# Kernel optimization log

Hardware: AMD Instinct MI355X
Metric: run time of the kernel (lower is better)

Reference implementation:

```python
import jax, jax.numpy as jnp
import numpy as np

H, D = 8, 16          # heads, per-head dim (hidden 128 = H*D)
IN_C, HID, OUT_C = 128, 128, 64
NG, ND = 100000, 50000
EG, EDG = 800000, 800000
NEG_SLOPE = 0.2


def setup_inputs() -> dict:
    key = jax.random.key(0)
    ks = jax.random.split(key, 20)
    inp = {}
    inp['x_gene'] = jax.random.normal(ks[0], (NG, IN_C), jnp.float32)
    inp['x_disease'] = jax.random.normal(ks[1], (ND, IN_C), jnp.float32)
    inp['eg_src'] = jax.random.randint(ks[2], (EG,), 0, NG, jnp.int32)
    inp['eg_dst'] = jax.random.randint(ks[3], (EG,), 0, NG, jnp.int32)
    inp['edg_src'] = jax.random.randint(ks[4], (EDG,), 0, ND, jnp.int32)
    inp['edg_dst'] = jax.random.randint(ks[5], (EDG,), 0, NG, jnp.int32)
    s = 1.0 / np.sqrt(IN_C)
    inp['W_gene'] = jax.random.normal(ks[6], (IN_C, HID), jnp.float32) * s
    inp['b_gene'] = jnp.zeros((HID,), jnp.float32)
    inp['W_dis'] = jax.random.normal(ks[7], (IN_C, HID), jnp.float32) * s
    inp['b_dis'] = jnp.zeros((HID,), jnp.float32)
    inp['att_src_gg'] = jax.random.normal(ks[8], (H, D), jnp.float32) * 0.1
    inp['att_dst_gg'] = jax.random.normal(ks[9], (H, D), jnp.float32) * 0.1
    inp['att_src_dg'] = jax.random.normal(ks[10], (H, D), jnp.float32) * 0.1
    inp['att_dst_dg'] = jax.random.normal(ks[11], (H, D), jnp.float32) * 0.1
    inp['Wk'] = jax.random.normal(ks[12], (HID, HID), jnp.float32) * (1.0 / np.sqrt(HID))
    inp['bk'] = jnp.zeros((HID,), jnp.float32)
    inp['q'] = jax.random.normal(ks[13], (HID,), jnp.float32) * 0.1
    inp['W_lin'] = jax.random.normal(ks[14], (HID, OUT_C), jnp.float32) * (1.0 / np.sqrt(HID))
    inp['b_lin'] = jnp.zeros((OUT_C,), jnp.float32)
    return inp


def _edge_attn(xs, xd, src, dst, a_s, a_d, n_dst):
    # xs:[Ns,H,D] projected src feats, xd:[Nd,H,D]; GAT-style per-edge-type attention
    e_src = (xs * a_s).sum(-1)                      # [Ns,H]
    e_dst = (xd * a_d).sum(-1)                      # [Nd,H]
    alpha = jax.nn.leaky_relu(e_src[src] + e_dst[dst], NEG_SLOPE)   # [E,H]
    m = jax.ops.segment_max(alpha, dst, num_segments=n_dst)
    m = jnp.where(jnp.isfinite(m), m, 0.0)
    ex = jnp.exp(alpha - m[dst])
    denom = jax.ops.segment_sum(ex, dst, num_segments=n_dst)
    w = ex / (denom[dst] + 1e-16)                   # softmax over incoming edges
    msg = xs[src] * w[..., None]                    # [E,H,D]
    out = jax.ops.segment_sum(msg, dst, num_segments=n_dst)  # [Nd,H,D]
    return jax.nn.relu(out.reshape(n_dst, H * D))


def reference(x_gene, x_disease, eg_src, eg_dst, edg_src, edg_dst,
              W_gene, b_gene, W_dis, b_dis,
              att_src_gg, att_dst_gg, att_src_dg, att_dst_dg,
              Wk, bk, q, W_lin, b_lin):
    ng = x_gene.shape[0]
    hg = (x_gene @ W_gene + b_gene).reshape(ng, H, D)
    hd = (x_disease @ W_dis + b_dis).reshape(-1, H, D)
    # metapath aggregations landing on 'gene'
    out_gg = _edge_attn(hg, hg, eg_src, eg_dst, att_src_gg, att_dst_gg, ng)
    out_dg = _edge_attn(hd, hg, edg_src, edg_dst, att_src_dg, att_dst_dg, ng)
    outs = jnp.stack([out_gg, out_dg])              # [K=2, Ng, HID]
    # semantic-level attention
    score = (jnp.tanh(outs @ Wk + bk).mean(1) * q).sum(-1)   # [K]
    beta = jax.nn.softmax(score)
    gene = (beta[:, None, None] * outs).sum(0)      # [Ng, HID]
    return gene @ W_lin + b_lin                     # [Ng, OUT_C]
```

## Files before the change

### kernel.cpp

```cpp
#include <hip/hip_runtime.h>
#include <cstdint>
#include <cstddef>

#define NEG_SLOPE 0.2f
#define BSHIFT 8

typedef __attribute__((ext_vector_type(8))) short short8;
typedef __attribute__((ext_vector_type(4))) float f32x4;

__device__ __forceinline__ float leakyf(float x) { return x > 0.f ? x : NEG_SLOPE * x; }
__device__ __forceinline__ float fast_tanh(float x) {
    float e = __expf(2.f * x);
    return 1.f - 2.f / (e + 1.f);
}
__device__ __forceinline__ unsigned short f2bf(float x) {
    unsigned u = __float_as_uint(x);
    unsigned r = u + 0x7FFFu + ((u >> 16) & 1u);
    return (unsigned short)(r >> 16);
}

__global__ __launch_bounds__(256) void proj_kernel(
    const float* __restrict__ x, const float* __restrict__ W, const float* __restrict__ bias,
    unsigned short* __restrict__ hout, int N,
    const float* __restrict__ att0, float* __restrict__ e0,
    const float* __restrict__ att1, float* __restrict__ e1,
    const float* __restrict__ att2, float* __restrict__ e2)
{
    __shared__ float xlds[32 * 128];
    __shared__ float wlds[16 * 128];
    const int t = threadIdx.x;
    const int row0 = blockIdx.x * 32;
    #pragma unroll
    for (int p = 0; p < 4; ++p) {
        int idx = t + 256 * p;
        int r = idx >> 5;
        int c4 = idx & 31;
        float4 v = make_float4(0.f, 0.f, 0.f, 0.f);
        if (row0 + r < N) v = *(const float4*)(x + (size_t)(row0 + r) * 128 + c4 * 4);
        *(float4*)(xlds + r * 128 + c4 * 4) = v;
    }
    const int rg = t >> 5, ct = t & 31;
    float acc[4][4];
    {
        float4 bv = *(const float4*)(bias + ct * 4);
        #pragma unroll
        for (int rr = 0; rr < 4; ++rr) {
            acc[rr][0] = bv.x; acc[rr][1] = bv.y; acc[rr][2] = bv.z; acc[rr][3] = bv.w;
        }
    }
    for (int kc = 0; kc < 8; ++kc) {
        __syncthreads();
        #pragma unroll
        for (int p = 0; p < 2; ++p) {
            int idx = t + 256 * p;
            *(float4*)(wlds + idx * 4) = *(const float4*)(W + (size_t)kc * 2048 + idx * 4);
        }
        __syncthreads();
        #pragma unroll 2
        for (int i2 = 0; i2 < 16; i2 += 4) {
            const int i = kc * 16 + i2;
            float4 xv[4];
            #pragma unroll
            for (int rr = 0; rr < 4; ++rr) xv[rr] = *(const float4*)(xlds + (rg + 8 * rr) * 128 + i);
            #pragma unroll
            for (int qq = 0; qq < 4; ++qq) {
                float4 wv = *(const float4*)(wlds + (i2 + qq) * 128 + ct * 4);
                #pragma unroll
                for (int rr = 0; rr < 4; ++rr) {
                    float xs = ((const float*)&xv[rr])[qq];
                    acc[rr][0] = fmaf(xs, wv.x, acc[rr][0]);
                    acc[rr][1] = fmaf(xs, wv.y, acc[rr][1]);
                    acc[rr][2] = fmaf(xs, wv.z, acc[rr][2]);
                    acc[rr][3] = fmaf(xs, wv.w, acc[rr][3]);
                }
            }
        }
    }
    #pragma unroll
    for (int rr = 0; rr < 4; ++rr) {
        int grow = row0 + rg + 8 * rr;
        if (grow < N) {
            int2 u;
            u.x = (int)f2bf(acc[rr][0]) | ((int)f2bf(acc[rr][1]) << 16);
            u.y = (int)f2bf(acc[rr][2]) | ((int)f2bf(acc[rr][3]) << 16);
            *(int2*)(hout + (size_t)grow * 128 + ct * 4) = u;
        }
    }
    const int head = ct >> 2;
    const bool wlane = (ct & 3) == 0;
    if (att0) {
        float4 av = *(const float4*)(att0 + ct * 4);
        #pragma unroll
        for (int rr = 0; rr < 4; ++rr) {
            float p_ = acc[rr][0] * av.x + acc[rr][1] * av.y + acc[rr][2] * av.z + acc[rr][3] * av.w;
            p_ += __shfl_xor(p_, 1);
            p_ += __shfl_xor(p_, 2);
            int grow = row0 + rg + 8 * rr;
            if (wlane && grow < N) e0[(size_t)grow * 8 + head] = p_;
        }
    }
    if (att1) {
        float4 av = *(const float4*)(att1 + ct * 4);
        #pragma unroll
        for (int rr = 0; rr < 4; ++rr) {
            float p_ = acc[rr][0] * av.x + acc[rr][1] * av.y + acc[rr][2] * av.z + acc[rr][3] * av.w;
            p_ += __shfl_xor(p_, 1);
            p_ += __shfl_xor(p_, 2);
            int grow = row0 + rg + 8 * rr;
            if (wlane && grow < N) e1[(size_t)grow * 8 + head] = p_;
        }
    }
    if (att2) {
        float4 av = *(const float4*)(att2 + ct * 4);
        #pragma unroll
        for (int rr = 0; rr < 4; ++rr) {
            float p_ = acc[rr][0] * av.x + acc[rr][1] * av.y + acc[rr][2] * av.z + acc[rr][3] * av.w;
            p_ += __shfl_xor(p_, 1);
            p_ += __shfl_xor(p_, 2);
            int grow = row0 + rg + 8 * rr;
            if (wlane && grow < N) e2[(size_t)grow * 8 + head] = p_;
        }
    }
}

__global__ __launch_bounds__(256) void bucket_hist(
    const int* __restrict__ dstg, int Eg, const int* __restrict__ dstd, int Ed,
    int NBg, int NBtot, int* __restrict__ bucketCnt)
{
    __shared__ int h[1024];
    const int t = threadIdx.x;
    for (int j = t; j < NBtot; j += 256) h[j] = 0;
    __syncthreads();
    const int Etot = Eg + Ed;
    const int base = blockIdx.x * 4096;
    #pragma unroll
    for (int k = 0; k < 16; ++k) {
        int i = base + k * 256 + t;
        if (i < Etot) {
            int b = (i < Eg) ? (dstg[i] >> BSHIFT) : NBg + (dstd[i - Eg] >> BSHIFT);
            atomicAdd(&h[b], 1);
        }
    }
    __syncthreads();
    for (int j = t; j < NBtot; j += 256) {
        int c = h[j];
        if (c) atomicAdd(&bucketCnt[j], c);
    }
}

__global__ void bucket_scan(const int* __restrict__ bucketCnt, int NBtot, int Etot,
                            int* __restrict__ bucketBase, int* __restrict__ bucketCursor)
{
    __shared__ int s[1024];
    int t = threadIdx.x;
    int v = (t < NBtot) ? bucketCnt[t] : 0;
    s[t] = v;
    __syncthreads();
    for (int o = 1; o < 1024; o <<= 1) {
        int add = (t >= o) ? s[t - o] : 0;
        __syncthreads();
        s[t] += add;
        __syncthreads();
    }
    if (t < NBtot) {
        int e = s[t] - v;
        bucketBase[t] = e;
        bucketCursor[t] = e;
    }
    if (t == 0) bucketBase[NBtot] = Etot;
}

__global__ __launch_bounds__(256) void bucket_scatter(
    const int* __restrict__ dstg, const int* __restrict__ srcg, int Eg,
    const int* __restrict__ dstd, const int* __restrict__ srcd, int Ed,
    int NBg, int NBtot, int* __restrict__ bucketCursor, unsigned* __restrict__ coarse)
{
    __shared__ int h[800];
    __shared__ int basearr[800];
    __shared__ int cur[800];
    const int t = threadIdx.x;
    for (int j = t; j < NBtot; j += 256) h[j] = 0;
    __syncthreads();
    const int Etot = Eg + Ed;
    const int base = blockIdx.x * 4096;
    int bk[16];
    unsigned pk[16];
    #pragma unroll
    for (int k = 0; k < 16; ++k) {
        int i = base + k * 256 + t;
        bk[k] = -1;
        if (i < Etot) {
            int dst, src, goff;
            if (i < Eg) { dst = dstg[i]; src = srcg[i]; goff = 0; }
            else        { dst = dstd[i - Eg]; src = srcd[i - Eg]; goff = NBg; }
            bk[k] = goff + (dst >> BSHIFT);
            pk[k] = (unsigned)src | ((unsigned)(dst & 255) << 24);
            atomicAdd(&h[bk[k]], 1);
        }
    }
    __syncthreads();
    for (int j = t; j < NBtot; j += 256) {
        int c = h[j];
        basearr[j] = c ? atomicAdd(&bucketCursor[j], c) : 0;
        cur[j] = 0;
    }
    __syncthreads();
    #pragma unroll
    for (int k = 0; k < 16; ++k) {
        if (bk[k] >= 0) {
            int r = atomicAdd(&cur[bk[k]], 1);
            coarse[basearr[bk[k]] + r] = pk[k];
        }
    }
}

__global__ __launch_bounds__(256) void bucket_sort(
    const unsigned* __restrict__ coarse, const int* __restrict__ bucketBase,
    int NBg, int Eg, int Ed, int N,
    int* __restrict__ offg, int* __restrict__ offd,
    int* __restrict__ srcs_g, int* __restrict__ srcs_d)
{
    __shared__ int hist[256];
    __shared__ int excl[256];
    __shared__ int cur[256];
    const int b = blockIdx.x;
    const int t = threadIdx.x;
    const int s0 = bucketBase[b], s1 = bucketBase[b + 1];
    const int cnt = s1 - s0;
    const bool isg = b < NBg;
    const int d0 = (isg ? b : b - NBg) << BSHIFT;
    hist[t] = 0;
    __syncthreads();
    for (int i = t; i < cnt; i += 256) {
        unsigned p = coarse[s0 + i];
        atomicAdd(&hist[p >> 24], 1);
    }
    __syncthreads();
    int v = hist[t];
    excl[t] = v;
    __syncthreads();
    for (int o = 1; o < 256; o <<= 1) {
        int add = (t >= o) ? excl[t - o] : 0;
        __syncthreads();
        excl[t] += add;
        __syncthreads();
    }
    const int e = excl[t] - v;
    const int localBase = isg ? s0 : s0 - Eg;
    const int d = d0 + t;
    if (d < N) {
        if (isg) offg[d] = localBase + e;
        else     offd[d] = localBase + e;
    }
    cur[t] = e;
    __syncthreads();
    int* outp = isg ? srcs_g : srcs_d;
    for (int i = t; i < cnt; i += 256) {
        unsigned p = coarse[s0 + i];
        int r = atomicAdd(&cur[p >> 24], 1);
        outp[localBase + r] = (int)(p & 0xFFFFFFu);
    }
    if (b == 0 && t == 0) { offg[N] = Eg; offd[N] = Ed; }
}

__global__ __launch_bounds__(256) void aggregate_kernel(
    const unsigned short* __restrict__ xs,
    const float* __restrict__ esrc,
    const float* __restrict__ edst,
    const int* __restrict__ off,
    const int* __restrict__ srcsorted,
    float* __restrict__ outp,
    int Nd)
{
    __shared__ float exbuf[4][64 * 8];
    const int lane = threadIdx.x & 63;
    const int wslot = threadIdx.x >> 6;
    const int n = blockIdx.x * 4 + wslot;
    if (n >= Nd) return;
    const int o0 = off[n], o1 = off[n + 1];
    const int deg = o1 - o0;
    const int li = lane & 31, half = lane >> 5;
    const int j0 = li * 4;
    const int hh = li >> 2;
    if (deg == 0) {
        if (half == 0) *(float4*)(outp + (size_t)n * 128 + j0) = make_float4(0.f, 0.f, 0.f, 0.f);
        return;
    }
    float ed[8];
    {
        float4 a = *(const float4*)(edst + (size_t)n * 8);
        float4 b = *(const float4*)(edst + (size_t)n * 8 + 4);
        ed[0] = a.x; ed[1] = a.y; ed[2] = a.z; ed[3] = a.w;
        ed[4] = b.x; ed[5] = b.y; ed[6] = b.z; ed[7] = b.w;
    }
    if (deg <= 64) {
        const bool act = lane < deg;
        int s = act ? srcsorted[o0 + lane] : 0;
        float exv[8];
        {
            float4 ea = make_float4(0.f, 0.f, 0.f, 0.f), eb = ea;
            if (act) {
                ea = *(const float4*)(esrc + (size_t)s * 8);
                eb = *(const float4*)(esrc + (size_t)s * 8 + 4);
            }
            float a[8] = {ea.x, ea.y, ea.z, ea.w, eb.x, eb.y, eb.z, eb.w};
            #pragma unroll
            for (int h2 = 0; h2 < 8; ++h2)
                exv[h2] = act ? __expf(leakyf(a[h2] + ed[h2])) : 0.f;
        }
        *(float4*)(&exbuf[wslot][lane * 8])     = make_float4(exv[0], exv[1], exv[2], exv[3]);
        *(float4*)(&exbuf[wslot][lane * 8 + 4]) = make_float4(exv[4], exv[5], exv[6], exv[7]);
        float4 num = make_float4(0.f, 0.f, 0.f, 0.f);
        float den = 0.f;
        const int iters = (deg + 1) >> 1;
        #pragma unroll 2
        for (int k = 0; k < iters; ++k) {
            int i = 2 * k + half;
            if (i < deg) {
                int si = __shfl(s, i);
                float wgt = exbuf[wslot][i * 8 + hh];
                int2 xv2 = *(const int2*)(xs + (size_t)si * 128 + j0);
                unsigned ux = (unsigned)xv2.x, uy = (unsigned)xv2.y;
                float x0 = __uint_as_float(ux << 16);
                float x1 = __uint_as_float(ux & 0xFFFF0000u);
                float x2 = __uint_as_float(uy << 16);
                float x3 = __uint_as_float(uy & 0xFFFF0000u);
                num.x = fmaf(wgt, x0, num.x);
                num.y = fmaf(wgt, x1, num.y);
                num.z = fmaf(wgt, x2, num.z);
                num.w = fmaf(wgt, x3, num.w);
                den += wgt;
            }
        }
        num.x += __shfl_xor(num.x, 32);
        num.y += __shfl_xor(num.y, 32);
        num.z += __shfl_xor(num.z, 32);
        num.w += __shfl_xor(num.w, 32);
        den += __shfl_xor(den, 32);
        if (half == 0) {
            float inv = 1.f / (den + 1e-16f);
            float4 r;
            r.x = fmaxf(num.x * inv, 0.f);
            r.y = fmaxf(num.y * inv, 0.f);
            r.z = fmaxf(num.z * inv, 0.f);
            r.w = fmaxf(num.w * inv, 0.f);
            *(float4*)(outp + (size_t)n * 128 + j0) = r;
        }
        return;
    }
    {
        const int j0b = lane * 2;
        const int h = lane >> 3;
        float edh;
        {
            float u4a = (h & 4) ? ed[4] : ed[0];
            float u4b = (h & 4) ? ed[5] : ed[1];
            float u4c = (h & 4) ? ed[6] : ed[2];
            float u4d = (h & 4) ? ed[7] : ed[3];
            float u2a = (h & 2) ? u4c : u4a;
            float u2b = (h & 2) ? u4d : u4b;
            edh = (h & 1) ? u2b : u2a;
        }
        float den = 0.f, num0 = 0.f, num1 = 0.f;
        for (int base = 0; base < deg; base += 64) {
            int ii = base + lane;
            bool act = ii < deg;
            int sreg = srcsorted[o0 + (act ? ii : 0)];
            int cl = deg - base;
            if (cl > 64) cl = 64;
            for (int i = 0; i < cl; ++i) {
                int s = __shfl(sreg, i);
                float ev = esrc[(size_t)s * 8 + h];
                float ex = __expf(leakyf(ev + edh));
                unsigned uv = *(const unsigned*)(xs + (size_t)s * 128 + j0b);
                float x0 = __uint_as_float(uv << 16);
                float x1 = __uint_as_float(uv & 0xFFFF0000u);
                num0 = fmaf(ex, x0, num0);
                num1 = fmaf(ex, x1, num1);
                den += ex;
            }
        }
        float inv = 1.f / (den + 1e-16f);
        float r0 = num0 * inv, r1 = num1 * inv;
        r0 = r0 > 0.f ? r0 : 0.f;
        r1 = r1 > 0.f ? r1 : 0.f;
        *(float2*)(outp + (size_t)n * 128 + j0b) = make_float2(r0, r1);
    }
}

__global__ void wkt_kernel(const float* __restrict__ Wk, unsigned short* __restrict__ WkT) {
    int c = threadIdx.x;
    for (int k = 0; k < 128; ++k)
        WkT[c * 128 + k] = f2bf(Wk[(size_t)k * 128 + c]);
}

__global__ __launch_bounds__(256) void score2_mfma(
    const float* __restrict__ gg, const float* __restrict__ dg,
    const unsigned short* __restrict__ WkT,
    const float* __restrict__ bk, const float* __restrict__ q,
    float* __restrict__ scoreAcc, int N)
{
    __shared__ short atile[128 * 128];
    __shared__ float sred[4];
    const int t = threadIdx.x;
    const int row0 = blockIdx.x * 64;
    {
        const int row = t >> 1, q8 = t & 1;
        const int gr = row0 + (row & 63);
        const float* srcp = (row < 64) ? gg : dg;
        #pragma unroll
        for (int c = 0; c < 8; ++c) {
            const int kc = q8 * 8 + c;
            float4 l0 = make_float4(0.f, 0.f, 0.f, 0.f), l1 = l0;
            if (gr < N) {
                l0 = *(const float4*)(srcp + (size_t)gr * 128 + kc * 8);
                l1 = *(const float4*)(srcp + (size_t)gr * 128 + kc * 8 + 4);
            }
            int4 u;
            u.x = (int)f2bf(l0.x) | ((int)f2bf(l0.y) << 16);
            u.y = (int)f2bf(l0.z) | ((int)f2bf(l0.w) << 16);
            u.z = (int)f2bf(l1.x) | ((int)f2bf(l1.y) << 16);
            u.w = (int)f2bf(l1.z) | ((int)f2bf(l1.w) << 16);
            const int chunk = row * 16 + kc;
            const int chunk_sw = chunk ^ (row & 7);
            *(int4*)((char*)atile + chunk_sw * 16) = u;
        }
    }
    __syncthreads();
    const int w = t >> 6, l = t & 63;
    const int lrow = l & 15, lk = l >> 4;
    f32x4 acc[2][8];
    #pragma unroll
    for (int a = 0; a < 2; ++a)
        #pragma unroll
        for (int ct = 0; ct < 8; ++ct) { acc[a][ct][0] = 0.f; acc[a][ct][1] = 0.f; acc[a][ct][2] = 0.f; acc[a][ct][3] = 0.f; }
    #pragma unroll
    for (int ks = 0; ks < 4; ++ks) {
        short8 afr[2];
        #pragma unroll
        for (int a = 0; a < 2; ++a) {
            const int rowl = w * 32 + a * 16 + lrow;
            const int chunk = rowl * 16 + ks * 4 + lk;
            const int chunk_sw = chunk ^ (rowl & 7);
            afr[a] = *(short8*)((char*)atile + chunk_sw * 16);
        }
        #pragma unroll
        for (int ct = 0; ct < 8; ++ct) {
            const unsigned short* bp = WkT + ((size_t)(ct * 16 + lrow) * 128 + ks * 32 + lk * 8);
            short8 bfr = *(const short8*)bp;
            acc[0][ct] = __builtin_amdgcn_mfma_f32_16x16x32_bf16(afr[0], bfr, acc[0][ct], 0, 0, 0);
            acc[1][ct] = __builtin_amdgcn_mfma_f32_16x16x32_bf16(afr[1], bfr, acc[1][ct], 0, 0, 0);
        }
    }
    float s = 0.f;
    #pragma unroll
    for (int ct = 0; ct < 8; ++ct) {
        const int col = ct * 16 + lrow;
        const float bkv = bk[col];
        const float qv = q[col];
        #pragma unroll
        for (int a = 0; a < 2; ++a) {
            #pragma unroll
            for (int r = 0; r < 4; ++r) {
                const int rloc = a * 16 + lk * 4 + r;
                const int grow = row0 + ((w * 32 + rloc) & 63);
                if (grow < N) s = fmaf(fast_tanh(acc[a][ct][r] + bkv), qv, s);
            }
        }
    }
    #pragma unroll
    for (int o = 1; o < 64; o <<= 1) s += __shfl_xor(s, o);
    if (l == 0) sred[w] = s;
    __syncthreads();
    if (t == 0) {
        float pg = sred[0] + sred[1];
        float pd = sred[2] + sred[3];
        int slot = blockIdx.x & 63;
        atomicAdd(&scoreAcc[slot], pg);
        atomicAdd(&scoreAcc[64 + slot], pd);
    }
}

__global__ void beta_kernel(float* __restrict__ scoreAcc, float invN) {
    int t = threadIdx.x;
    float v0 = scoreAcc[t];
    float v1 = scoreAcc[64 + t];
    #pragma unroll
    for (int o = 1; o < 64; o <<= 1) {
        v0 += __shfl_xor(v0, o);
        v1 += __shfl_xor(v1, o);
    }
    if (t == 0) {
        float s0 = v0 * invN, s1 = v1 * invN;
        float mx = fmaxf(s0, s1);
        float e0 = __expf(s0 - mx), e1 = __expf(s1 - mx);
        float inv = 1.f / (e0 + e1);
        scoreAcc[128] = e0 * inv;
        scoreAcc[129] = e1 * inv;
    }
}

__global__ __launch_bounds__(256) void final_kernel(
    const float* __restrict__ gg, const float* __restrict__ dg,
    const float* __restrict__ beta,
    const float* __restrict__ Wl, const float* __restrict__ bl,
    float* __restrict__ outp, int N)
{
    __shared__ float wlds[128 * 64];
    __shared__ float glds[32 * 128];
    const int t = threadIdx.x;
    #pragma unroll
    for (int p = 0; p < 8; ++p) {
        int idx = (t + 256 * p) * 4;
        *(float4*)(wlds + idx) = *(const float4*)(Wl + idx);
    }
    const float bet0 = beta[0], bet1 = beta[1];
    const int row0 = blockIdx.x * 32;
    #pragma unroll
    for (int p = 0; p < 4; ++p) {
        int idx = t + 256 * p;
        int r = idx >> 5;
        int c4 = idx & 31;
        float4 a = make_float4(0.f, 0.f, 0.f, 0.f), b = a, g;
        if (row0 + r < N) {
            a = *(const float4*)(gg + (size_t)(row0 + r) * 128 + c4 * 4);
            b = *(const float4*)(dg + (size_t)(row0 + r) * 128 + c4 * 4);
        }
        g.x = bet0 * a.x + bet1 * b.x;
        g.y = bet0 * a.y + bet1 * b.y;
        g.z = bet0 * a.z + bet1 * b.z;
        g.w = bet0 * a.w + bet1 * b.w;
        *(float4*)(glds + r * 128 + c4 * 4) = g;
    }
    __syncthreads();
    const int rg = t >> 5, ct = t & 31;
    float acc[4][2];
    {
        float2 bv = *(const float2*)(bl + ct * 2);
        #pragma unroll
        for (int rr = 0; rr < 4; ++rr) { acc[rr][0] = bv.x; acc[rr][1] = bv.y; }
    }
    #pragma unroll 2
    for (int i = 0; i < 128; i += 4) {
        float4 xv[4];
        #pragma unroll
        for (int rr = 0; rr < 4; ++rr) xv[rr] = *(const float4*)(glds + (rg + 8 * rr) * 128 + i);
        #pragma unroll
        for (int qq = 0; qq < 4; ++qq) {
            float2 wv = *(const float2*)(wlds + (i + qq) * 64 + ct * 2);
            #pragma unroll
            for (int rr = 0; rr < 4; ++rr) {
                float xs = ((const float*)&xv[rr])[qq];
                acc[rr][0] = fmaf(xs, wv.x, acc[rr][0]);
                acc[rr][1] = fmaf(xs, wv.y, acc[rr][1]);
            }
        }
    }
    #pragma unroll
    for (int rr = 0; rr < 4; ++rr) {
        int grow = row0 + rg + 8 * rr;
        if (grow < N)
            *(float2*)(outp + (size_t)grow * 64 + ct * 2) = make_float2(acc[rr][0], acc[rr][1]);
    }
}

extern "C" void kernel_launch(void* const* d_in, const int* in_sizes, int n_in,
                              void* d_out, int out_size, void* d_ws, size_t ws_size,
                              hipStream_t stream) {
    (void)n_in; (void)out_size; (void)ws_size;
    const float* x_gene = (const float*)d_in[0];
    const float* x_dis  = (const float*)d_in[1];
    const int* eg_src   = (const int*)d_in[2];
    const int* eg_dst   = (const int*)d_in[3];
    const int* edg_src  = (const int*)d_in[4];
    const int* edg_dst  = (const int*)d_in[5];
    const float* W_gene = (const float*)d_in[6];
    const float* b_gene = (const float*)d_in[7];
    const float* W_dis  = (const float*)d_in[8];
    const float* b_dis  = (const float*)d_in[9];
    const float* att_src_gg = (const float*)d_in[10];
    const float* att_dst_gg = (const float*)d_in[11];
    const float* att_src_dg = (const float*)d_in[12];
    const float* att_dst_dg = (const float*)d_in[13];
    const float* Wk    = (const float*)d_in[14];
    const float* bk    = (const float*)d_in[15];
    const float* q     = (const float*)d_in[16];
    const float* W_lin = (const float*)d_in[17];
    const float* b_lin = (const float*)d_in[18];
    float* out = (float*)d_out;

    const int NG_ = in_sizes[0] / 128;
    const int ND_ = in_sizes[1] / 128;
    const int EG_ = in_sizes[2];
    const int EDG_ = in_sizes[4];

    char* w = (char*)d_ws;
    auto alloc = [&](size_t bytes) -> char* {
        char* p = w;
        w += (bytes + 255) & ~(size_t)255;
        return p;
    };
    unsigned short* hg = (unsigned short*)alloc((size_t)NG_ * 128 * 2);
    unsigned short* hd = (unsigned short*)alloc((size_t)ND_ * 128 * 2);
    float* e_src_gg = (float*)alloc((size_t)NG_ * 8 * 4);
    float* e_dst_gg = (float*)alloc((size_t)NG_ * 8 * 4);
    float* e_dst_dg = (float*)alloc((size_t)NG_ * 8 * 4);
    float* e_src_dg = (float*)alloc((size_t)ND_ * 8 * 4);
    float* out_gg   = (float*)alloc((size_t)NG_ * 128 * 4);
    float* out_dg   = (float*)alloc((size_t)NG_ * 128 * 4);
    int* offg  = (int*)alloc((size_t)(NG_ + 1) * 4);
    int* offd  = (int*)alloc((size_t)(NG_ + 1) * 4);
    int* srcs_g = (int*)alloc((size_t)EG_ * 4);
    int* srcs_d = (int*)alloc((size_t)EDG_ * 4);
    unsigned* coarse = (unsigned*)alloc((size_t)(EG_ + EDG_) * 4);
    int* bucketCnt    = (int*)alloc(4096);
    int* bucketBase   = (int*)alloc(4096);
    int* bucketCursor = (int*)alloc(4096);
    unsigned short* WkT = (unsigned short*)alloc(128 * 128 * 2);
    float* score = (float*)alloc(1024);

    const int NBg = (NG_ + 255) >> BSHIFT;
    const int NBtot = 2 * NBg;
    const int Etot = EG_ + EDG_;
    const int nbE = (Etot + 4095) / 4096;

    proj_kernel<<<(NG_ + 31) / 32, 256, 0, stream>>>(
        x_gene, W_gene, b_gene, hg, NG_,
        att_src_gg, e_src_gg, att_dst_gg, e_dst_gg, att_dst_dg, e_dst_dg);
    proj_kernel<<<(ND_ + 31) / 32, 256, 0, stream>>>(
        x_dis, W_dis, b_dis, hd, ND_,
        att_src_dg, e_src_dg, (const float*)nullptr, (float*)nullptr,
        (const float*)nullptr, (float*)nullptr);
    wkt_kernel<<<1, 128, 0, stream>>>(Wk, WkT);

    hipMemsetAsync(bucketCnt, 0, (size_t)NBtot * 4, stream);
    bucket_hist<<<nbE, 256, 0, stream>>>(eg_dst, EG_, edg_dst, EDG_, NBg, NBtot, bucketCnt);
    bucket_scan<<<1, 1024, 0, stream>>>(bucketCnt, NBtot, Etot, bucketBase, bucketCursor);
    bucket_scatter<<<nbE, 256, 0, stream>>>(
        eg_dst, eg_src, EG_, edg_dst, edg_src, EDG_, NBg, NBtot, bucketCursor, coarse);
    bucket_sort<<<NBtot, 256, 0, stream>>>(
        coarse, bucketBase, NBg, EG_, EDG_, NG_, offg, offd, srcs_g, srcs_d);

    aggregate_kernel<<<(NG_ + 3) / 4, 256, 0, stream>>>(
        hg, e_src_gg, e_dst_gg, offg, srcs_g, out_gg, NG_);
    aggregate_kernel<<<(NG_ + 3) / 4, 256, 0, stream>>>(
        hd, e_src_dg, e_dst_dg, offd, srcs_d, out_dg, NG_);

    hipMemsetAsync(score, 0, 512, stream);
    score2_mfma<<<(NG_ + 63) / 64, 256, 0, stream>>>(out_gg, out_dg, WkT, bk, q, score, NG_);
    beta_kernel<<<1, 64, 0, stream>>>(score, 1.0f / (float)NG_);

    final_kernel<<<(NG_ + 31) / 32, 256, 0, stream>>>(
        out_gg, out_dg, score + 128, W_lin, b_lin, out, NG_);
}
```

Baseline: 377.9 us.

## Replace FP32 projection with bf16 MFMA GEMM folding attention logits as extra columns

```diff
diff --git a/kernel.cpp b/kernel.cpp
--- a/kernel.cpp
+++ b/kernel.cpp
@@ -19,106 +19,132 @@
     return (unsigned short)(r >> 16);
 }
 
-__global__ __launch_bounds__(256) void proj_kernel(
-    const float* __restrict__ x, const float* __restrict__ W, const float* __restrict__ bias,
-    unsigned short* __restrict__ hout, int N,
-    const float* __restrict__ att0, float* __restrict__ e0,
-    const float* __restrict__ att1, float* __restrict__ e1,
-    const float* __restrict__ att2, float* __restrict__ e2)
-{
-    __shared__ float xlds[32 * 128];
-    __shared__ float wlds[16 * 128];
+__global__ void bext_kernel(const float* __restrict__ W, const float* __restrict__ bias,
+                            const float* __restrict__ att0, const float* __restrict__ att1,
+                            const float* __restrict__ att2,
+                            unsigned short* __restrict__ BExt, float* __restrict__ beArr)
+{
     const int t = threadIdx.x;
-    const int row0 = blockIdx.x * 32;
-    #pragma unroll
-    for (int p = 0; p < 4; ++p) {
-        int idx = t + 256 * p;
-        int r = idx >> 5;
-        int c4 = idx & 31;
-        float4 v = make_float4(0.f, 0.f, 0.f, 0.f);
-        if (row0 + r < N) v = *(const float4*)(x + (size_t)(row0 + r) * 128 + c4 * 4);
-        *(float4*)(xlds + r * 128 + c4 * 4) = v;
-    }
-    const int rg = t >> 5, ct = t & 31;
-    float acc[4][4];
+    for (int task = t; task < 128 * 128; task += 256) {
+        int col = task >> 7, k = task & 127;
+        BExt[(size_t)col * 128 + k] = f2bf(W[(size_t)k * 128 + col]);
+    }
+    for (int task = t; task < 32 * 128; task += 256) {
+        int col = task >> 7, k = task & 127;
+        int vec = col >> 3, h = col & 7;
+        const float* att = (vec == 0) ? att0 : (vec == 1) ? att1 : (vec == 2) ? att2 : nullptr;
+        float s = 0.f;
+        if (att) {
+            #pragma unroll
+            for (int d = 0; d < 16; ++d) s = fmaf(W[(size_t)k * 128 + h * 16 + d], att[h * 16 + d], s);
+        }
+        BExt[(size_t)(128 + col) * 128 + k] = f2bf(s);
+    }
+    if (t < 24) {
+        int vec = t >> 3, h = t & 7;
+        const float* att = (vec == 0) ? att0 : (vec == 1) ? att1 : att2;
+        float s = 0.f;
+        if (att) {
+            #pragma unroll
+            for (int d = 0; d < 16; ++d) s = fmaf(bias[h * 16 + d], att[h * 16 + d], s);
+        }
+        beArr[t] = s;
+    }
+}
+
+__global__ __launch_bounds__(256) void proj_mfma(
+    const float* __restrict__ x, const unsigned short* __restrict__ BExt,
+    const float* __restrict__ bias, const float* __restrict__ beArr,
+    unsigned short* __restrict__ hout,
+    float* __restrict__ e0, float* __restrict__ e1, float* __restrict__ e2, int N)
+{
+    __shared__ short atile[128 * 128];
+    const int t = threadIdx.x;
+    const int row0 = blockIdx.x * 128;
     {
-        float4 bv = *(const float4*)(bias + ct * 4);
-        #pragma unroll
-        for (int rr = 0; rr < 4; ++rr) {
-            acc[rr][0] = bv.x; acc[rr][1] = bv.y; acc[rr][2] = bv.z; acc[rr][3] = bv.w;
-        }
-    }
-    for (int kc = 0; kc < 8; ++kc) {
-        __syncthreads();
-        #pragma unroll
-        for (int p = 0; p < 2; ++p) {
-            int idx = t + 256 * p;
-            *(float4*)(wlds + idx * 4) = *(const float4*)(W + (size_t)kc * 2048 + idx * 4);
-        }
-        __syncthreads();
-        #pragma unroll 2
-        for (int i2 = 0; i2 < 16; i2 += 4) {
-            const int i = kc * 16 + i2;
-            float4 xv[4];
-            #pragma unroll
-            for (int rr = 0; rr < 4; ++rr) xv[rr] = *(const float4*)(xlds + (rg + 8 * rr) * 128 + i);
-            #pragma unroll
-            for (int qq = 0; qq < 4; ++qq) {
-                float4 wv = *(const float4*)(wlds + (i2 + qq) * 128 + ct * 4);
+        const int row = t >> 1, q8 = t & 1;
+        const int gr = row0 + row;
+        #pragma unroll
+        for (int c = 0; c < 8; ++c) {
+            const int kc = q8 * 8 + c;
+            float4 l0 = make_float4(0.f, 0.f, 0.f, 0.f), l1 = l0;
+            if (gr < N) {
+                l0 = *(const float4*)(x + (size_t)gr * 128 + kc * 8);
+                l1 = *(const float4*)(x + (size_t)gr * 128 + kc * 8 + 4);
+            }
+            int4 u;
+            u.x = (int)f2bf(l0.x) | ((int)f2bf(l0.y) << 16);
+            u.y = (int)f2bf(l0.z) | ((int)f2bf(l0.w) << 16);
+            u.z = (int)f2bf(l1.x) | ((int)f2bf(l1.y) << 16);
+            u.w = (int)f2bf(l1.z) | ((int)f2bf(l1.w) << 16);
+            const int chunk = row * 16 + kc;
+            const int chunk_sw = chunk ^ (row & 7);
+            *(int4*)((char*)atile + chunk_sw * 16) = u;
+        }
+    }
+    __syncthreads();
+    const int w = t >> 6, l = t & 63;
+    const int lrow = l & 15, lk = l >> 4;
+    f32x4 acc[2][10];
+    #pragma unroll
+    for (int a = 0; a < 2; ++a)
+        #pragma unroll
+        for (int ct = 0; ct < 10; ++ct) { acc[a][ct][0] = 0.f; acc[a][ct][1] = 0.f; acc[a][ct][2] = 0.f; acc[a][ct][3] = 0.f; }
+    #pragma unroll
+    for (int ks = 0; ks < 4; ++ks) {
+        short8 afr[2];
+        #pragma unroll
+        for (int a = 0; a < 2; ++a) {
+            const int rowl = w * 32 + a * 16 + lrow;
+            const int chunk = rowl * 16 + ks * 4 + lk;
+            const int chunk_sw = chunk ^ (rowl & 7);
+            afr[a] = *(short8*)((char*)atile + chunk_sw * 16);
+        }
+        #pragma unroll
+        for (int ct = 0; ct < 10; ++ct) {
+            const unsigned short* bp = BExt + ((size_t)(ct * 16 + lrow) * 128 + ks * 32 + lk * 8);
+            short8 bfr = *(const short8*)bp;
+            acc[0][ct] = __builtin_amdgcn_mfma_f32_16x16x32_bf16(afr[0], bfr, acc[0][ct], 0, 0, 0);
+            acc[1][ct] = __builtin_amdgcn_mfma_f32_16x16x32_bf16(afr[1], bfr, acc[1][ct], 0, 0, 0);
+        }
+    }
+    #pragma unroll
+    for (int ct = 0; ct < 8; ++ct) {
+        const int col = ct * 16 + lrow;
+        const float bv = bias[col];
+        #pragma unroll
+        for (int a = 0; a < 2; ++a) {
+            #pragma unroll
+            for (int r = 0; r < 4; ++r) {
+                const int grow = row0 + w * 32 + a * 16 + lk * 4 + r;
+                if (grow < N) hout[(size_t)grow * 128 + col] = f2bf(acc[a][ct][r] + bv);
+            }
+        }
+    }
+    {
+        const float be = beArr[lrow];
+        float* tgt = (lrow < 8) ? e0 : e1;
+        const int head = lrow & 7;
+        if (tgt) {
+            #pragma unroll
+            for (int a = 0; a < 2; ++a) {
                 #pragma unroll
-                for (int rr = 0; rr < 4; ++rr) {
-                    float xs = ((const float*)&xv[rr])[qq];
-                    acc[rr][0] = fmaf(xs, wv.x, acc[rr][0]);
-                    acc[rr][1] = fmaf(xs, wv.y, acc[rr][1]);
-                    acc[rr][2] = fmaf(xs, wv.z, acc[rr][2]);
-                    acc[rr][3] = fmaf(xs, wv.w, acc[rr][3]);
+                for (int r = 0; r < 4; ++r) {
+                    const int grow = row0 + w * 32 + a * 16 + lk * 4 + r;
+                    if (grow < N) tgt[(size_t)grow * 8 + head] = acc[a][8][r] + be;
                 }
             }
         }
     }
-    #pragma unroll
-    for (int rr = 0; rr < 4; ++rr) {
-        int grow = row0 + rg + 8 * rr;
-        if (grow < N) {
-            int2 u;
-            u.x = (int)f2bf(acc[rr][0]) | ((int)f2bf(acc[rr][1]) << 16);
-            u.y = (int)f2bf(acc[rr][2]) | ((int)f2bf(acc[rr][3]) << 16);
-            *(int2*)(hout + (size_t)grow * 128 + ct * 4) = u;
-        }
-    }
-    const int head = ct >> 2;
-    const bool wlane = (ct & 3) == 0;
-    if (att0) {
-        float4 av = *(const float4*)(att0 + ct * 4);
-        #pragma unroll
-        for (int rr = 0; rr < 4; ++rr) {
-            float p_ = acc[rr][0] * av.x + acc[rr][1] * av.y + acc[rr][2] * av.z + acc[rr][3] * av.w;
-            p_ += __shfl_xor(p_, 1);
-            p_ += __shfl_xor(p_, 2);
-            int grow = row0 + rg + 8 * rr;
-            if (wlane && grow < N) e0[(size_t)grow * 8 + head] = p_;
-        }
-    }
-    if (att1) {
-        float4 av = *(const float4*)(att1 + ct * 4);
-        #pragma unroll
-        for (int rr = 0; rr < 4; ++rr) {
-            float p_ = acc[rr][0] * av.x + acc[rr][1] * av.y + acc[rr][2] * av.z + acc[rr][3] * av.w;
-            p_ += __shfl_xor(p_, 1);
-            p_ += __shfl_xor(p_, 2);
-            int grow = row0 + rg + 8 * rr;
-            if (wlane && grow < N) e1[(size_t)grow * 8 + head] = p_;
-        }
-    }
-    if (att2) {
-        float4 av = *(const float4*)(att2 + ct * 4);
-        #pragma unroll
-        for (int rr = 0; rr < 4; ++rr) {
-            float p_ = acc[rr][0] * av.x + acc[rr][1] * av.y + acc[rr][2] * av.z + acc[rr][3] * av.w;
-            p_ += __shfl_xor(p_, 1);
-            p_ += __shfl_xor(p_, 2);
-            int grow = row0 + rg + 8 * rr;
-            if (wlane && grow < N) e2[(size_t)grow * 8 + head] = p_;
+    if (lrow < 8 && e2) {
+        const float be = beArr[16 + lrow];
+        #pragma unroll
+        for (int a = 0; a < 2; ++a) {
+            #pragma unroll
+            for (int r = 0; r < 4; ++r) {
+                const int grow = row0 + w * 32 + a * 16 + lk * 4 + r;
+                if (grow < N) e2[(size_t)grow * 8 + lrow] = acc[a][9][r] + be;
+            }
         }
     }
 }
@@ -616,7 +642,11 @@
     int* bucketCnt    = (int*)alloc(4096);
     int* bucketBase   = (int*)alloc(4096);
     int* bucketCursor = (int*)alloc(4096);
-    unsigned short* WkT = (unsigned short*)alloc(128 * 128 * 2);
+    unsigned short* WkT   = (unsigned short*)alloc(128 * 128 * 2);
+    unsigned short* bextg = (unsigned short*)alloc(160 * 128 * 2);
+    unsigned short* bextd = (unsigned short*)alloc(160 * 128 * 2);
+    float* beg = (float*)alloc(128);
+    float* bed = (float*)alloc(128);
     float* score = (float*)alloc(1024);
 
     const int NBg = (NG_ + 255) >> BSHIFT;
@@ -624,14 +654,16 @@
     const int Etot = EG_ + EDG_;
     const int nbE = (Etot + 4095) / 4096;
 
-    proj_kernel<<<(NG_ + 31) / 32, 256, 0, stream>>>(
-        x_gene, W_gene, b_gene, hg, NG_,
-        att_src_gg, e_src_gg, att_dst_gg, e_dst_gg, att_dst_dg, e_dst_dg);
-    proj_kernel<<<(ND_ + 31) / 32, 256, 0, stream>>>(
-        x_dis, W_dis, b_dis, hd, ND_,
-        att_src_dg, e_src_dg, (const float*)nullptr, (float*)nullptr,
-        (const float*)nullptr, (float*)nullptr);
+    bext_kernel<<<1, 256, 0, stream>>>(W_gene, b_gene,
+        att_src_gg, att_dst_gg, att_dst_dg, bextg, beg);
+    bext_kernel<<<1, 256, 0, stream>>>(W_dis, b_dis,
+        att_src_dg, (const float*)nullptr, (const float*)nullptr, bextd, bed);
     wkt_kernel<<<1, 128, 0, stream>>>(Wk, WkT);
+
+    proj_mfma<<<(NG_ + 127) / 128, 256, 0, stream>>>(
+        x_gene, bextg, b_gene, beg, hg, e_src_gg, e_dst_gg, e_dst_dg, NG_);
+    proj_mfma<<<(ND_ + 127) / 128, 256, 0, stream>>>(
+        x_dis, bextd, b_dis, bed, hd, e_src_dg, (float*)nullptr, (float*)nullptr, ND_);
 
     hipMemsetAsync(bucketCnt, 0, (size_t)NBtot * 4, stream);
     bucket_hist<<<nbE, 256, 0, stream>>>(eg_dst, EG_, edg_dst, EDG_, NBg, NBtot, bucketCnt);
```

Result: slower. 413.4 us (+9.4%).
